# Kernel optimization log

Measured on AMD Instinct MI355X. Metric: run time of the kernel, lower is better.

Reference implementation:

```python
import jax, jax.numpy as jnp
import numpy as np
from jax import lax

B, L, V = 128, 64, 8192
E = H = 128
STEPS = 10
MAX_BIN = 512
BETA_START, BETA_END = 1e-4, 2e-2


def setup_inputs():
    key = jax.random.key(0)
    k = jax.random.split(key, 23)
    s = 0.05
    padded_x = (jax.random.uniform(k[0], (B, L, V)) < 0.01).astype(jnp.float32)
    lengths = jax.random.randint(k[1], (B,), 1, L + 1)
    visit_mask = (jnp.arange(L)[None, :] < lengths[:, None]).astype(jnp.float32)
    padded_bins = jnp.sort(jax.random.randint(k[2], (B, L), 0, MAX_BIN), axis=1)
    t_diff = jax.random.randint(k[3], (B,), 1, STEPS + 1)
    eps = jax.random.normal(k[4], (B, L, E))
    z0 = jax.random.normal(k[5], (B, L, E))
    noise = jax.random.normal(k[6], (STEPS, B, L, E))
    W_visit = jax.random.normal(k[7], (E, V)) * s
    bin_embed = (jax.random.normal(k[8], (MAX_BIN + 2, E)) * s).at[0].set(0.0)  # padding_idx=0
    W_ih = jax.random.normal(k[9], (4 * H, E)) * s
    W_hh = jax.random.normal(k[10], (4 * H, H)) * s
    b_ih = jax.random.normal(k[11], (4 * H,)) * s
    b_hh = jax.random.normal(k[12], (4 * H,)) * s
    W_cls = jax.random.normal(k[13], (1, H)) * s
    b_cls = jax.random.normal(k[14], (1,)) * s
    W_proj = jax.random.normal(k[15], (E, H)) * s
    time_embed = jax.random.normal(k[16], (STEPS + 1, E)) * s
    W_fuse = jax.random.normal(k[17], (2, 2 * E)) * s
    b_fuse = jax.random.normal(k[18], (2,)) * s
    W_e1 = jax.random.normal(k[19], (E, 2 * E)) * s
    b_e1 = jax.random.normal(k[20], (E,)) * s
    W_e2 = jax.random.normal(k[21], (E, E)) * s
    b_e2 = jax.random.normal(k[22], (E,)) * s
    return dict(padded_x=padded_x, visit_mask=visit_mask, padded_bins=padded_bins,
                t_diff=t_diff, eps=eps, z0=z0, noise=noise, W_visit=W_visit,
                bin_embed=bin_embed, W_ih=W_ih, W_hh=W_hh, b_ih=b_ih, b_hh=b_hh,
                W_cls=W_cls, b_cls=b_cls, W_proj=W_proj, time_embed=time_embed,
                W_fuse=W_fuse, b_fuse=b_fuse, W_e1=W_e1, b_e1=b_e1, W_e2=W_e2, b_e2=b_e2)


def _lstm(v, W_ih, W_hh, b_ih, b_hh):
    # v: [B,L,E] -> h: [B,L,H]; PyTorch gate order i,f,g,o
    xg = jnp.einsum('ble,ge->blg', v, W_ih) + b_ih + b_hh
    def step(carry, x):
        h, c = carry
        g = x + h @ W_hh.T
        i, f, gg, o = jnp.split(g, 4, axis=-1)
        c = jax.nn.sigmoid(f) * c + jax.nn.sigmoid(i) * jnp.tanh(gg)
        h = jax.nn.sigmoid(o) * jnp.tanh(c)
        return (h, c), h
    z = jnp.zeros((v.shape[0], W_hh.shape[1]), v.dtype)
    _, hs = lax.scan(step, (z, z), jnp.swapaxes(xg, 0, 1))
    return jnp.swapaxes(hs, 0, 1)


def _last_hidden(h, mask):
    lengths = jnp.maximum(mask.sum(axis=1).astype(jnp.int32), 1)
    return h[jnp.arange(h.shape[0]), lengths - 1]


def reference(padded_x, visit_mask, padded_bins, t_diff, eps, z0, noise,
              W_visit, bin_embed, W_ih, W_hh, b_ih, b_hh, W_cls, b_cls,
              W_proj, time_embed, W_fuse, b_fuse, W_e1, b_e1, W_e2, b_e2):
    m = visit_mask[..., None]                      # [B,L,1]
    betas = jnp.linspace(BETA_START, BETA_END, STEPS)
    alphas = 1.0 - betas
    alpha_bars = jnp.cumprod(alphas)

    # visit embedding + time-gap (delta bin) embedding
    delta = jnp.concatenate([jnp.zeros_like(padded_bins[:, :1]),
                             jnp.clip(padded_bins[:, 1:] - padded_bins[:, :-1], 0)], axis=1)
    delta = jnp.where(visit_mask > 0, jnp.clip(delta, 0, MAX_BIN + 1), 0)
    v = (padded_x @ W_visit.T + bin_embed[delta]) * m  # [B,L,E]

    # encoder LSTM (packed seq == plain scan then zero padded suffix positions)
    h = _lstm(v, W_ih, W_hh, b_ih, b_hh) * m
    logits_real = (_last_hidden(h, visit_mask) @ W_cls.T + b_cls)[:, 0]

    h_prev = jnp.pad(h[:, :-1], ((0, 0), (1, 0), (0, 0)))
    hp = (h_prev @ W_proj.T) * m                   # [B,L,E]

    def fuse_eps(z, t_emb):
        a = jax.nn.softmax(jnp.concatenate([z, hp], -1) @ W_fuse.T + b_fuse, axis=-1)
        g = a[..., :1] * z + a[..., 1:] * hp
        x = jnp.concatenate([g, t_emb], -1)
        return jax.nn.relu(x @ W_e1.T + b_e1) @ W_e2.T + b_e2

    # diffusion loss
    t = jnp.where(visit_mask > 0, t_diff[:, None], 1)    # [B,L]
    ab = alpha_bars[t - 1][..., None]
    z_t = (jnp.sqrt(ab) * v + jnp.sqrt(1.0 - ab) * eps) * m
    eps_pred = fuse_eps(z_t, time_embed[t])
    denom = jnp.maximum(visit_mask.sum(), 1.0)
    diffusion_loss = jnp.sum((eps_pred - eps) ** 2 * m) / denom

    # reverse diffusion sampling of synthetic visit embeddings
    def step(z, inp):
        kk, nz = inp
        t_s = jnp.where(visit_mask > 0, kk, 1)
        e = fuse_eps(z, time_embed[t_s])
        beta = betas[kk - 1]
        mean = (z - beta / jnp.sqrt(1.0 - alpha_bars[kk - 1]) * e) / jnp.sqrt(alphas[kk - 1])
        z = jnp.where(kk > 1, mean + jnp.sqrt(beta) * nz, mean) * m
        return z, None

    ks = jnp.arange(STEPS, 0, -1)
    v_syn, _ = lax.scan(step, z0, (ks, noise))

    h_syn = _lstm(v_syn, W_ih, W_hh, b_ih, b_hh) * m
    logits_syn = (_last_hidden(h_syn, visit_mask) @ W_cls.T + b_cls)[:, 0]
    return logits_real, logits_syn, diffusion_loss
```

## Files before the change

kernel.cpp:

```cpp
#include <hip/hip_runtime.h>

#define B_ 128
#define L_ 64
#define V_ 8192
#define E_ 128
#define H_ 128
#define G4_ 512
#define NROW (B_*L_)
#define HSTRIDE 136
#define AS 136
#define XS 264
#define YS 136
#define ZS 132

typedef unsigned short u16;
typedef __attribute__((ext_vector_type(8))) short bf16x8;
typedef __attribute__((ext_vector_type(4))) float f32x4;

__device__ __forceinline__ float sigm(float x){ return 1.f/(1.f + __expf(-x)); }
__device__ __forceinline__ float ftanh(float x){ float e = __expf(2.f*x); return 1.f - 2.f/(e + 1.f); }
__device__ __forceinline__ u16 f2bf(float f){
    union { unsigned int i; float f; } x; x.f = f;
    unsigned int r = x.i + 0x7fff + ((x.i >> 16) & 1);
    return (u16)(r >> 16);
}
#define LBAR() asm volatile("s_waitcnt lgkmcnt(0)\ns_barrier" ::: "memory")

__device__ __forceinline__ bf16x8 pack8(const float* p){
    const float4* q = (const float4*)p;
    float4 a = q[0], b = q[1];
    bf16x8 f;
    f[0]=(short)f2bf(a.x); f[1]=(short)f2bf(a.y); f[2]=(short)f2bf(a.z); f[3]=(short)f2bf(a.w);
    f[4]=(short)f2bf(b.x); f[5]=(short)f2bf(b.y); f[6]=(short)f2bf(b.z); f[7]=(short)f2bf(b.w);
    return f;
}

__global__ __launch_bounds__(256) void k_transpose_wv(const float* __restrict__ Wv, float* __restrict__ WT){
    __shared__ float tile[16][129];
    int v0 = blockIdx.x * 16;
    int t = threadIdx.x;
    #pragma unroll
    for(int i=0;i<8;i++){
        int idx = i*256 + t; int e = idx >> 4; int vv = idx & 15;
        tile[vv][e] = Wv[(size_t)e*V_ + v0 + vv];
    }
    __syncthreads();
    #pragma unroll
    for(int i=0;i<8;i++){
        int idx = i*256 + t; int vv = idx >> 7; int e = idx & 127;
        WT[(size_t)(v0+vv)*E_ + e] = tile[vv][e];
    }
}

__global__ __launch_bounds__(256) void k_visit_embed(const float* __restrict__ px, const float* __restrict__ vmask,
                                                     const int* __restrict__ bins, const float* __restrict__ bemb,
                                                     const float* __restrict__ WT, float* __restrict__ v){
    __shared__ int idxs[512];
    __shared__ int cnt;
    __shared__ int dsh;
    __shared__ float msh;
    __shared__ float4 red[8][32];
    int row = blockIdx.x; int l = row & 63;
    int t = threadIdx.x;
    if(t==0){
        cnt = 0;
        float m = vmask[row];
        int d = 0;
        if(l > 0){ d = bins[row] - bins[row-1]; d = d < 0 ? 0 : (d > 513 ? 513 : d); }
        if(!(m > 0.f)) d = 0;
        dsh = d; msh = m;
    }
    __syncthreads();
    const uint4* xr4 = (const uint4*)(px + (size_t)row * V_);
    for(int i=t;i<2048;i+=256){
        uint4 u = xr4[i];
        unsigned int w[4] = {u.x,u.y,u.z,u.w};
        #pragma unroll
        for(int j=0;j<4;j++){
            if(w[j]){ int p = atomicAdd(&cnt,1); if(p<512) idxs[p] = i*4 + j; }
        }
    }
    __syncthreads();
    int n = cnt; if(n > 512) n = 512;
    int eq = t & 31, jg = t >> 5;
    float4 a4 = {0.f,0.f,0.f,0.f};
    for(int j=jg;j<n;j+=8){
        const float4* wr = (const float4*)(WT + (size_t)idxs[j]*E_);
        float4 wv = wr[eq];
        a4.x += wv.x; a4.y += wv.y; a4.z += wv.z; a4.w += wv.w;
    }
    red[jg][eq] = a4;
    __syncthreads();
    if(t < 32){
        float4 s = red[0][t];
        #pragma unroll
        for(int g=1;g<8;g++){
            float4 r = red[g][t];
            s.x += r.x; s.y += r.y; s.z += r.z; s.w += r.w;
        }
        const float4* bp = (const float4*)(bemb + dsh*E_);
        float4 bv = bp[t];
        float m = msh;
        float4 o;
        o.x = (s.x + bv.x)*m; o.y = (s.y + bv.y)*m; o.z = (s.z + bv.z)*m; o.w = (s.w + bv.w)*m;
        ((float4*)(v + (size_t)row*E_))[t] = o;
    }
}

__global__ __launch_bounds__(256,2) void k_gemm_xg(const float* __restrict__ A, const float* __restrict__ Wih,
                                                   const float* __restrict__ bih, const float* __restrict__ bhh,
                                                   float* __restrict__ xg){
    __shared__ __align__(16) u16 abuf[16*AS];
    int t = threadIdx.x, wave = t >> 6, lane = t & 63, quad = lane >> 4, lc = lane & 15;
    int row0 = blockIdx.x * 16;
    #pragma unroll
    for(int i=0;i<8;i++){
        int flat = i*256 + t; int r = flat >> 7, e = flat & 127;
        abuf[r*AS + e] = f2bf(A[(size_t)(row0+r)*E_ + e]);
    }
    bf16x8 wfr[8][4]; float bb[8];
    #pragma unroll
    for(int nt=0;nt<8;nt++){
        int n = wave*128 + nt*16 + lc;
        bb[nt] = bih[n] + bhh[n];
        const float* wr = Wih + (size_t)n*E_ + quad*8;
        #pragma unroll
        for(int kt=0;kt<4;kt++) wfr[nt][kt] = pack8(wr + kt*32);
    }
    __syncthreads();
    f32x4 acc[8];
    #pragma unroll
    for(int nt=0;nt<8;nt++) acc[nt] = (f32x4){0.f,0.f,0.f,0.f};
    #pragma unroll
    for(int kt=0;kt<4;kt++){
        bf16x8 af = *(const bf16x8*)&abuf[lc*AS + kt*32 + quad*8];
        #pragma unroll
        for(int nt=0;nt<8;nt++)
            acc[nt] = __builtin_amdgcn_mfma_f32_16x16x32_bf16(af, wfr[nt][kt], acc[nt], 0,0,0);
    }
    #pragma unroll
    for(int nt=0;nt<8;nt++){
        int n = wave*128 + nt*16 + lc;
        #pragma unroll
        for(int r=0;r<4;r++)
            xg[(size_t)(row0 + quad*4 + r)*G4_ + n] = acc[nt][r] + bb[nt];
    }
}

__device__ __forceinline__ void lstm_step(int l, const float* pxg, float* hp_out, bool dohp,
        const u16* bufr, u16* bufw, const bf16x8 (&bf)[4][4], const bf16x8 (&wp)[4],
        float (&xgbuf)[4][4], float (&c4)[4], float (&lg4)[4],
        const int (&len4)[4], float wcv,
        const float* vmsh, int lc, int quad, int wave, int b0){
    float xloc[4][4];
    #pragma unroll
    for(int gate=0;gate<4;gate++){
        #pragma unroll
        for(int r=0;r<4;r++) xloc[gate][r] = xgbuf[gate][r];
    }
    if(l+2 < 64){
        #pragma unroll
        for(int gate=0;gate<4;gate++){
            #pragma unroll
            for(int r=0;r<4;r++)
                xgbuf[gate][r] = pxg[(size_t)r*64*G4_ + (size_t)(l+2)*G4_ + gate*128];
        }
    }
    bf16x8 af[4];
    #pragma unroll
    for(int kt=0;kt<4;kt++)
        af[kt] = *(const bf16x8*)&bufr[lc*HSTRIDE + kt*32 + quad*8];
    f32x4 acc[4], acch;
    #pragma unroll
    for(int a=0;a<4;a++) acc[a] = (f32x4){0.f,0.f,0.f,0.f};
    acch = (f32x4){0.f,0.f,0.f,0.f};
    #pragma unroll
    for(int kt=0;kt<4;kt++){
        #pragma unroll
        for(int a=0;a<4;a++)
            acc[a] = __builtin_amdgcn_mfma_f32_16x16x32_bf16(af[kt], bf[a][kt], acc[a], 0,0,0);
        acch = __builtin_amdgcn_mfma_f32_16x16x32_bf16(af[kt], wp[kt], acch, 0,0,0);
    }
    if(dohp){
        #pragma unroll
        for(int r=0;r<4;r++){
            float m = vmsh[(quad*4+r)*64 + l];
            int grow = (b0 + quad*4 + r)*64 + l;
            hp_out[(size_t)grow*E_ + wave*16 + lc] = acch[r] * m;
        }
    }
    #pragma unroll
    for(int r=0;r<4;r++){
        float gi = acc[0][r] + xloc[0][r];
        float gf = acc[1][r] + xloc[1][r];
        float gg = acc[2][r] + xloc[2][r];
        float go = acc[3][r] + xloc[3][r];
        float c  = sigm(gf)*c4[r] + sigm(gi)*ftanh(gg);
        float h  = sigm(go)*ftanh(c);
        c4[r] = c;
        bufw[(quad*4+r)*HSTRIDE + wave*16 + lc] = f2bf(h);
        if(l == len4[r]-1) lg4[r] += h * wcv;
    }
    LBAR();
}

__global__ __launch_bounds__(512,2) void k_lstm_fused(const float* __restrict__ xg, const float* __restrict__ Whh,
        const float* __restrict__ Wproj, const float* __restrict__ Wcls, const float* __restrict__ bcls,
        const float* __restrict__ vmask, float* __restrict__ hp_out, float* __restrict__ logits_out){
    __shared__ u16 hbuf[2][16*HSTRIDE];
    __shared__ float vmsh[16*64];
    __shared__ int lensh[16];
    __shared__ float lgsh[16][132];
    int t = threadIdx.x;
    int wave = t >> 6, lane = t & 63;
    int quad = lane >> 4, lc = lane & 15;
    int b0 = blockIdx.x * 16;
    bool dohp = (hp_out != nullptr);

    for(int i=t;i<16*HSTRIDE;i+=512) hbuf[0][i] = 0;
    for(int i=t;i<1024;i+=512) vmsh[i] = vmask[b0*64 + i];
    __syncthreads();
    if(t < 16){
        int s = 0;
        #pragma unroll
        for(int i=0;i<64;i++) s += (vmsh[t*64 + i] > 0.f) ? 1 : 0;
        lensh[t] = s < 1 ? 1 : s;
    }

    int cw = wave*16 + lc;
    bf16x8 bf[4][4];
    #pragma unroll
    for(int gate=0;gate<4;gate++){
        int n = gate*128 + cw;
        const float* wr = Whh + (size_t)n*H_ + quad*8;
        #pragma unroll
        for(int kt=0;kt<4;kt++) bf[gate][kt] = pack8(wr + kt*32);
    }
    bf16x8 wp[4];
    {
        const float* wr = Wproj + (size_t)cw*H_ + quad*8;
        #pragma unroll
        for(int kt=0;kt<4;kt++) wp[kt] = pack8(wr + kt*32);
    }
    float wcv = Wcls[cw];

    float c4[4] = {0.f,0.f,0.f,0.f};
    float lg4[4] = {0.f,0.f,0.f,0.f};

    const float* pxg = xg + ((size_t)(b0 + quad*4))*64*G4_ + cw;

    float xgvE[4][4], xgvO[4][4];
    #pragma unroll
    for(int gate=0;gate<4;gate++){
        #pragma unroll
        for(int r=0;r<4;r++){
            xgvE[gate][r] = pxg[(size_t)r*64*G4_ + gate*128];
            xgvO[gate][r] = pxg[(size_t)r*64*G4_ + G4_ + gate*128];
        }
    }
    __syncthreads();
    int len4[4];
    #pragma unroll
    for(int r=0;r<4;r++) len4[r] = lensh[quad*4 + r];

    for(int lb=0;lb<64;lb+=2){
        lstm_step(lb,   pxg, hp_out, dohp, hbuf[0], hbuf[1], bf, wp, xgvE, c4, lg4, len4, wcv, vmsh, lc, quad, wave, b0);
        lstm_step(lb+1, pxg, hp_out, dohp, hbuf[1], hbuf[0], bf, wp, xgvO, c4, lg4, len4, wcv, vmsh, lc, quad, wave, b0);
    }
    #pragma unroll
    for(int r=0;r<4;r++) lgsh[quad*4+r][cw] = lg4[r];
    __syncthreads();
    {
        int row = t >> 5, l32 = t & 31;
        float s = lgsh[row][l32] + lgsh[row][l32+32] + lgsh[row][l32+64] + lgsh[row][l32+96];
        s += __shfl_down(s, 16, 32);
        s += __shfl_down(s, 8, 32);
        s += __shfl_down(s, 4, 32);
        s += __shfl_down(s, 2, 32);
        s += __shfl_down(s, 1, 32);
        if(l32 == 0) logits_out[b0 + row] = s + bcls[0];
    }
}

__global__ __launch_bounds__(256,2) void k_drg(const float* __restrict__ v, const float* __restrict__ hp,
        const float* __restrict__ eps, const int* __restrict__ tdiff, const float* __restrict__ vmask,
        const float* __restrict__ z0, const float* __restrict__ noise, const float* __restrict__ temb,
        const float* __restrict__ Wf, const float* __restrict__ bfu,
        const float* __restrict__ We1, const float* __restrict__ be1,
        const float* __restrict__ We2, const float* __restrict__ be2,
        const float* __restrict__ Wih, const float* __restrict__ bih, const float* __restrict__ bhh,
        float* __restrict__ partial, float* __restrict__ xg2){
    __shared__ float zbuf[16*ZS], hpbuf[16*ZS];
    __shared__ __align__(16) u16 xbuf[16*XS];
    __shared__ __align__(16) u16 y1buf[16*YS];
    __shared__ float wfsh[512];
    __shared__ float ssh[16][2], hpd[16][2];
    __shared__ float mrow[16]; __shared__ int trow[16];
    __shared__ float sbeta[10], sabar[10];
    __shared__ float rb[4];
    int row0 = blockIdx.x * 16; int t = threadIdx.x;
    int wave = t >> 6, lane = t & 63, quad = lane >> 4, lc = lane & 15;

    if(t==0){
        float p = 1.f;
        for(int k=0;k<10;k++){ float b = 1e-4f + (0.02f - 1e-4f)*k/9.f; sbeta[k] = b; p *= (1.f - b); sabar[k] = p; }
    }
    if(t < 16){
        int row = row0 + t; float m = vmask[row];
        mrow[t] = m; trow[t] = (m > 0.f) ? tdiff[row >> 6] : 1;
    }
    for(int i=t;i<512;i+=256) wfsh[i] = Wf[i];
    float z0reg[8];
    #pragma unroll
    for(int i=0;i<8;i++){
        int flat = i*256 + t; int r = flat >> 7; int e = flat & 127;
        z0reg[i] = z0[(size_t)(row0+r)*E_ + e];
    }
    __syncthreads();
    #pragma unroll
    for(int i=0;i<8;i++){
        int flat = i*256 + t; int r = flat >> 7; int e = flat & 127; int row = row0 + r;
        float ab = sabar[trow[r]-1];
        zbuf[r*ZS + e] = (sqrtf(ab)*v[(size_t)row*E_ + e] + sqrtf(1.f - ab)*eps[(size_t)row*E_ + e]) * mrow[r];
        hpbuf[r*ZS + e] = hp[(size_t)row*E_ + e];
    }
    bf16x8 wf1[2][8], wf2[2][4];
    float be1v[2], be2v[2];
    #pragma unroll
    for(int nt=0;nt<2;nt++){
        int n = wave*32 + nt*16 + lc;
        be1v[nt] = be1[n]; be2v[nt] = be2[n];
        const float* w1 = We1 + (size_t)n*256 + quad*8;
        #pragma unroll
        for(int kt=0;kt<8;kt++) wf1[nt][kt] = pack8(w1 + kt*32);
        const float* w2 = We2 + (size_t)n*128 + quad*8;
        #pragma unroll
        for(int kt=0;kt<4;kt++) wf2[nt][kt] = pack8(w2 + kt*32);
    }
    __syncthreads();
    {
        int row = t >> 4, k = (t >> 3) & 1, sub = t & 7;
        float p = 0.f;
        #pragma unroll
        for(int i=0;i<16;i++)
            p += hpbuf[row*ZS + sub*16 + i] * wfsh[k*256 + 128 + sub*16 + i];
        p += __shfl_down(p,4); p += __shfl_down(p,2); p += __shfl_down(p,1);
        if(sub == 0) hpd[row][k] = p + bfu[k];
    }
    LBAR();

    for(int s=0;s<11;s++){
        int kk = 10 - (s - 1);
        float nzreg[2][4];
        if(s >= 1){
            #pragma unroll
            for(int nt=0;nt<2;nt++){
                #pragma unroll
                for(int r=0;r<4;r++)
                    nzreg[nt][r] = noise[((size_t)(s-1)*NROW + row0 + quad*4 + r)*E_ + wave*32 + nt*16 + lc];
            }
        }
        {
            int row = t >> 4, k = (t >> 3) & 1, sub = t & 7;
            float q = 0.f;
            #pragma unroll
            for(int i=0;i<16;i++)
                q += zbuf[row*ZS + sub*16 + i] * wfsh[k*256 + sub*16 + i];
            q += __shfl_down(q,4); q += __shfl_down(q,2); q += __shfl_down(q,1);
            if(sub == 0) ssh[row][k] = q + hpd[row][k];
        }
        LBAR();
        {
            int row = t >> 4, c0 = (t & 15) * 16;
            float s0 = ssh[row][0], s1 = ssh[row][1];
            float a0 = 1.f/(1.f + __expf(s1 - s0)), a1 = 1.f - a0;
            int tt = (s == 0) ? trow[row] : ((mrow[row] > 0.f) ? kk : 1);
            #pragma unroll
            for(int i=0;i<16;i++){
                int c = c0 + i;
                float val = (c < 128) ? (a0*zbuf[row*ZS + c] + a1*hpbuf[row*ZS + c])
                                      : temb[tt*E_ + (c - 128)];
                xbuf[row*XS + c] = f2bf(val);
            }
        }
        LBAR();
        f32x4 acc1[2];
        acc1[0] = (f32x4){0.f,0.f,0.f,0.f}; acc1[1] = (f32x4){0.f,0.f,0.f,0.f};
        #pragma unroll
        for(int kt=0;kt<8;kt++){
            bf16x8 af = *(const bf16x8*)&xbuf[lc*XS + kt*32 + quad*8];
            acc1[0] = __builtin_amdgcn_mfma_f32_16x16x32_bf16(af, wf1[0][kt], acc1[0], 0,0,0);
            acc1[1] = __builtin_amdgcn_mfma_f32_16x16x32_bf16(af, wf1[1][kt], acc1[1], 0,0,0);
        }
        #pragma unroll
        for(int nt=0;nt<2;nt++){
            #pragma unroll
            for(int r=0;r<4;r++)
                y1buf[(quad*4+r)*YS + wave*32 + nt*16 + lc] = f2bf(fmaxf(acc1[nt][r] + be1v[nt], 0.f));
        }
        LBAR();
        f32x4 acc2[2];
        acc2[0] = (f32x4){0.f,0.f,0.f,0.f}; acc2[1] = (f32x4){0.f,0.f,0.f,0.f};
        #pragma unroll
        for(int kt=0;kt<4;kt++){
            bf16x8 af = *(const bf16x8*)&y1buf[lc*YS + kt*32 + quad*8];
            acc2[0] = __builtin_amdgcn_mfma_f32_16x16x32_bf16(af, wf2[0][kt], acc2[0], 0,0,0);
            acc2[1] = __builtin_amdgcn_mfma_f32_16x16x32_bf16(af, wf2[1][kt], acc2[1], 0,0,0);
        }
        if(s == 0){
            float lp = 0.f;
            #pragma unroll
            for(int nt=0;nt<2;nt++){
                int n = wave*32 + nt*16 + lc;
                #pragma unroll
                for(int r=0;r<4;r++){
                    int m = quad*4 + r;
                    float d = (acc2[nt][r] + be2v[nt]) - eps[(size_t)(row0+m)*E_ + n];
                    lp += d*d*mrow[m];
                }
            }
            #pragma unroll
            for(int off=32;off;off>>=1) lp += __shfl_down(lp, off);
            if(lane == 0) rb[wave] = lp;
            LBAR();
            if(t == 0) partial[blockIdx.x] = rb[0]+rb[1]+rb[2]+rb[3];
            #pragma unroll
            for(int i=0;i<8;i++){
                int flat = i*256 + t; int r = flat >> 7; int e = flat & 127;
                zbuf[r*ZS + e] = z0reg[i];
            }
            LBAR();
        } else {
            float beta = sbeta[kk-1];
            float c1 = beta / sqrtf(1.f - sabar[kk-1]);
            float c2 = 1.f / sqrtf(1.f - beta);
            float sb = sqrtf(beta);
            #pragma unroll
            for(int nt=0;nt<2;nt++){
                int n = wave*32 + nt*16 + lc;
                #pragma unroll
                for(int r=0;r<4;r++){
                    int m = quad*4 + r;
                    float e = acc2[nt][r] + be2v[nt];
                    float z = zbuf[m*ZS + n];
                    float mean = (z - c1*e) * c2;
                    float znew = (kk > 1) ? (mean + sb*nzreg[nt][r]) : mean;
                    zbuf[m*ZS + n] = znew * mrow[m];
                }
            }
            LBAR();
        }
    }
    {
        int row = t >> 4, c0 = (t & 15) * 8;
        #pragma unroll
        for(int i=0;i<8;i++)
            xbuf[row*XS + c0 + i] = f2bf(zbuf[row*ZS + c0 + i]);
    }
    bf16x8 wg[8][4]; float bb[8];
    #pragma unroll
    for(int nt=0;nt<8;nt++){
        int n = wave*128 + nt*16 + lc;
        bb[nt] = bih[n] + bhh[n];
        const float* wr = Wih + (size_t)n*E_ + quad*8;
        #pragma unroll
        for(int kt=0;kt<4;kt++) wg[nt][kt] = pack8(wr + kt*32);
    }
    LBAR();
    f32x4 ac[8];
    #pragma unroll
    for(int nt=0;nt<8;nt++) ac[nt] = (f32x4){0.f,0.f,0.f,0.f};
    #pragma unroll
    for(int kt=0;kt<4;kt++){
        bf16x8 af = *(const bf16x8*)&xbuf[lc*XS + kt*32 + quad*8];
        #pragma unroll
        for(int nt=0;nt<8;nt++)
            ac[nt] = __builtin_amdgcn_mfma_f32_16x16x32_bf16(af, wg[nt][kt], ac[nt], 0,0,0);
    }
    #pragma unroll
    for(int nt=0;nt<8;nt++){
        int n = wave*128 + nt*16 + lc;
        #pragma unroll
        for(int r=0;r<4;r++)
            xg2[(size_t)(row0 + quad*4 + r)*G4_ + n] = ac[nt][r] + bb[nt];
    }
}

__global__ void k_finalize(const float* __restrict__ partial, const float* __restrict__ vmask, float* __restrict__ out){
    __shared__ float rb[4], rl[4];
    int t = threadIdx.x;
    float s = 0.f;
    for(int i=t;i<NROW;i+=256) s += vmask[i];
    float ls = 0.f;
    for(int i=t;i<512;i+=256) ls += partial[i];
    #pragma unroll
    for(int off=32;off;off>>=1){ s += __shfl_down(s, off); ls += __shfl_down(ls, off); }
    if((t & 63) == 0){ rb[t >> 6] = s; rl[t >> 6] = ls; }
    __syncthreads();
    if(t == 0){
        float denom = rb[0]+rb[1]+rb[2]+rb[3];
        if(denom < 1.f) denom = 1.f;
        out[256] = (rl[0]+rl[1]+rl[2]+rl[3]) / denom;
    }
}

extern "C" void kernel_launch(void* const* d_in, const int* in_sizes, int n_in,
                              void* d_out, int out_size, void* d_ws, size_t ws_size,
                              hipStream_t stream){
    const float* px    = (const float*)d_in[0];
    const float* vmask = (const float*)d_in[1];
    const int*   bins  = (const int*)d_in[2];
    const int*   tdiff = (const int*)d_in[3];
    const float* eps   = (const float*)d_in[4];
    const float* z0    = (const float*)d_in[5];
    const float* noise = (const float*)d_in[6];
    const float* Wv    = (const float*)d_in[7];
    const float* bemb  = (const float*)d_in[8];
    const float* Wih   = (const float*)d_in[9];
    const float* Whh   = (const float*)d_in[10];
    const float* bih   = (const float*)d_in[11];
    const float* bhh   = (const float*)d_in[12];
    const float* Wcls  = (const float*)d_in[13];
    const float* bcls  = (const float*)d_in[14];
    const float* Wproj = (const float*)d_in[15];
    const float* temb  = (const float*)d_in[16];
    const float* Wf    = (const float*)d_in[17];
    const float* bfu   = (const float*)d_in[18];
    const float* We1   = (const float*)d_in[19];
    const float* be1   = (const float*)d_in[20];
    const float* We2   = (const float*)d_in[21];
    const float* be2   = (const float*)d_in[22];
    float* out = (float*)d_out;

    float* ws      = (float*)d_ws;
    float* WT      = ws;
    float* v       = ws + 1048576;
    float* xg      = ws + 2097152;
    float* hp      = ws + 6291456;
    float* partial = ws + 7340032;

    hipLaunchKernelGGL(k_transpose_wv, dim3(V_/16), dim3(256), 0, stream, Wv, WT);
    hipLaunchKernelGGL(k_visit_embed, dim3(NROW), dim3(256), 0, stream, px, vmask, bins, bemb, WT, v);
    hipLaunchKernelGGL(k_gemm_xg, dim3(NROW/16), dim3(256), 0, stream, v, Wih, bih, bhh, xg);
    hipLaunchKernelGGL(k_lstm_fused, dim3(B_/16), dim3(512), 0, stream,
                       xg, Whh, Wproj, Wcls, bcls, vmask, hp, out);
    hipLaunchKernelGGL(k_drg, dim3(NROW/16), dim3(256), 0, stream,
                       v, hp, eps, tdiff, vmask, z0, noise, temb, Wf, bfu,
                       We1, be1, We2, be2, Wih, bih, bhh, partial, xg);
    hipLaunchKernelGGL(k_lstm_fused, dim3(B_/16), dim3(512), 0, stream,
                       xg, Whh, Wproj, Wcls, bcls, vmask, (float*)nullptr, out + 128);
    hipLaunchKernelGGL(k_finalize, dim3(1), dim3(256), 0, stream, partial, vmask, out);
}
```

Measured before the change: 833.4 us.

## Split LSTM recurrence into 4-sequence blocks and store gate preactivations in bf16

The sequential LSTM kernel now assigns 4 batch sequences per block instead of 16, so it launches 32 blocks instead of 8. Each block still runs the 16-row MFMA, but only quad 0 does the gate math and writes results, leaving 12 of the 16 rows as zero padding. This trades wasted MFMA rows for more parallelism in a latency-bound recurrence. Separately, the input-gate preactivations xg are written and read as bf16 rather than fp32, halving that traffic at some cost in accuracy.

```diff
diff --git a/kernel.cpp b/kernel.cpp
--- a/kernel.cpp
+++ b/kernel.cpp
@@ -23,6 +23,9 @@
     union { unsigned int i; float f; } x; x.f = f;
     unsigned int r = x.i + 0x7fff + ((x.i >> 16) & 1);
     return (u16)(r >> 16);
+}
+__device__ __forceinline__ float bf2f(u16 u){
+    union { unsigned int i; float f; } x; x.i = ((unsigned int)u) << 16; return x.f;
 }
 #define LBAR() asm volatile("s_waitcnt lgkmcnt(0)\ns_barrier" ::: "memory")
 
@@ -109,7 +112,7 @@
 
 __global__ __launch_bounds__(256,2) void k_gemm_xg(const float* __restrict__ A, const float* __restrict__ Wih,
                                                    const float* __restrict__ bih, const float* __restrict__ bhh,
-                                                   float* __restrict__ xg){
+                                                   u16* __restrict__ xg){
     __shared__ __align__(16) u16 abuf[16*AS];
     int t = threadIdx.x, wave = t >> 6, lane = t & 63, quad = lane >> 4, lc = lane & 15;
     int row0 = blockIdx.x * 16;
@@ -143,15 +146,15 @@
         int n = wave*128 + nt*16 + lc;
         #pragma unroll
         for(int r=0;r<4;r++)
-            xg[(size_t)(row0 + quad*4 + r)*G4_ + n] = acc[nt][r] + bb[nt];
-    }
-}
-
-__device__ __forceinline__ void lstm_step(int l, const float* pxg, float* hp_out, bool dohp,
+            xg[(size_t)(row0 + quad*4 + r)*G4_ + n] = f2bf(acc[nt][r] + bb[nt]);
+    }
+}
+
+__device__ __forceinline__ void lstm_step(int l, int b0, const u16* __restrict__ xg, float* hp_out, bool dohp,
         const u16* bufr, u16* bufw, const bf16x8 (&bf)[4][4], const bf16x8 (&wp)[4],
         float (&xgbuf)[4][4], float (&c4)[4], float (&lg4)[4],
         const int (&len4)[4], float wcv,
-        const float* vmsh, int lc, int quad, int wave, int b0){
+        const float* vmsh, int lc, int quad, int cw){
     float xloc[4][4];
     #pragma unroll
     for(int gate=0;gate<4;gate++){
@@ -163,7 +166,7 @@
         for(int gate=0;gate<4;gate++){
             #pragma unroll
             for(int r=0;r<4;r++)
-                xgbuf[gate][r] = pxg[(size_t)r*64*G4_ + (size_t)(l+2)*G4_ + gate*128];
+                xgbuf[gate][r] = bf2f(xg[(size_t)((b0+r)*64 + l+2)*G4_ + gate*128 + cw]);
         }
     }
     bf16x8 af[4];
@@ -181,46 +184,43 @@
             acc[a] = __builtin_amdgcn_mfma_f32_16x16x32_bf16(af[kt], bf[a][kt], acc[a], 0,0,0);
         acch = __builtin_amdgcn_mfma_f32_16x16x32_bf16(af[kt], wp[kt], acch, 0,0,0);
     }
-    if(dohp){
+    if(quad == 0){
         #pragma unroll
         for(int r=0;r<4;r++){
-            float m = vmsh[(quad*4+r)*64 + l];
-            int grow = (b0 + quad*4 + r)*64 + l;
-            hp_out[(size_t)grow*E_ + wave*16 + lc] = acch[r] * m;
-        }
-    }
-    #pragma unroll
-    for(int r=0;r<4;r++){
-        float gi = acc[0][r] + xloc[0][r];
-        float gf = acc[1][r] + xloc[1][r];
-        float gg = acc[2][r] + xloc[2][r];
-        float go = acc[3][r] + xloc[3][r];
-        float c  = sigm(gf)*c4[r] + sigm(gi)*ftanh(gg);
-        float h  = sigm(go)*ftanh(c);
-        c4[r] = c;
-        bufw[(quad*4+r)*HSTRIDE + wave*16 + lc] = f2bf(h);
-        if(l == len4[r]-1) lg4[r] += h * wcv;
+            float m = vmsh[r*64 + l];
+            if(dohp)
+                hp_out[(size_t)((b0+r)*64 + l)*E_ + cw] = acch[r] * m;
+            float gi = acc[0][r] + xloc[0][r];
+            float gf = acc[1][r] + xloc[1][r];
+            float gg = acc[2][r] + xloc[2][r];
+            float go = acc[3][r] + xloc[3][r];
+            float c  = sigm(gf)*c4[r] + sigm(gi)*ftanh(gg);
+            float h  = sigm(go)*ftanh(c);
+            c4[r] = c;
+            bufw[r*HSTRIDE + cw] = f2bf(h);
+            if(l == len4[r]-1) lg4[r] += h * wcv;
+        }
     }
     LBAR();
 }
 
-__global__ __launch_bounds__(512,2) void k_lstm_fused(const float* __restrict__ xg, const float* __restrict__ Whh,
+__global__ __launch_bounds__(512,2) void k_lstm_fused(const u16* __restrict__ xg, const float* __restrict__ Whh,
         const float* __restrict__ Wproj, const float* __restrict__ Wcls, const float* __restrict__ bcls,
         const float* __restrict__ vmask, float* __restrict__ hp_out, float* __restrict__ logits_out){
     __shared__ u16 hbuf[2][16*HSTRIDE];
-    __shared__ float vmsh[16*64];
-    __shared__ int lensh[16];
-    __shared__ float lgsh[16][132];
+    __shared__ float vmsh[4*64];
+    __shared__ int lensh[4];
+    __shared__ float lgsh[4][132];
     int t = threadIdx.x;
     int wave = t >> 6, lane = t & 63;
     int quad = lane >> 4, lc = lane & 15;
-    int b0 = blockIdx.x * 16;
+    int b0 = blockIdx.x * 4;
     bool dohp = (hp_out != nullptr);
 
-    for(int i=t;i<16*HSTRIDE;i+=512) hbuf[0][i] = 0;
-    for(int i=t;i<1024;i+=512) vmsh[i] = vmask[b0*64 + i];
-    __syncthreads();
-    if(t < 16){
+    for(int i=t;i<2*16*HSTRIDE;i+=512) ((u16*)hbuf)[i] = 0;
+    for(int i=t;i<256;i+=512) vmsh[i] = vmask[b0*64 + i];
+    __syncthreads();
+    if(t < 4){
         int s = 0;
         #pragma unroll
         for(int i=0;i<64;i++) s += (vmsh[t*64 + i] > 0.f) ? 1 : 0;
@@ -247,30 +247,30 @@
     float c4[4] = {0.f,0.f,0.f,0.f};
     float lg4[4] = {0.f,0.f,0.f,0.f};
 
-    const float* pxg = xg + ((size_t)(b0 + quad*4))*64*G4_ + cw;
-
     float xgvE[4][4], xgvO[4][4];
     #pragma unroll
     for(int gate=0;gate<4;gate++){
         #pragma unroll
         for(int r=0;r<4;r++){
-            xgvE[gate][r] = pxg[(size_t)r*64*G4_ + gate*128];
-            xgvO[gate][r] = pxg[(size_t)r*64*G4_ + G4_ + gate*128];
+            xgvE[gate][r] = bf2f(xg[(size_t)((b0+r)*64 + 0)*G4_ + gate*128 + cw]);
+            xgvO[gate][r] = bf2f(xg[(size_t)((b0+r)*64 + 1)*G4_ + gate*128 + cw]);
         }
     }
     __syncthreads();
     int len4[4];
     #pragma unroll
-    for(int r=0;r<4;r++) len4[r] = lensh[quad*4 + r];
+    for(int r=0;r<4;r++) len4[r] = lensh[r];
 
     for(int lb=0;lb<64;lb+=2){
-        lstm_step(lb,   pxg, hp_out, dohp, hbuf[0], hbuf[1], bf, wp, xgvE, c4, lg4, len4, wcv, vmsh, lc, quad, wave, b0);
-        lstm_step(lb+1, pxg, hp_out, dohp, hbuf[1], hbuf[0], bf, wp, xgvO, c4, lg4, len4, wcv, vmsh, lc, quad, wave, b0);
-    }
-    #pragma unroll
-    for(int r=0;r<4;r++) lgsh[quad*4+r][cw] = lg4[r];
-    __syncthreads();
-    {
+        lstm_step(lb,   b0, xg, hp_out, dohp, hbuf[0], hbuf[1], bf, wp, xgvE, c4, lg4, len4, wcv, vmsh, lc, quad, cw);
+        lstm_step(lb+1, b0, xg, hp_out, dohp, hbuf[1], hbuf[0], bf, wp, xgvO, c4, lg4, len4, wcv, vmsh, lc, quad, cw);
+    }
+    if(quad == 0){
+        #pragma unroll
+        for(int r=0;r<4;r++) lgsh[r][cw] = lg4[r];
+    }
+    __syncthreads();
+    if(t < 128){
         int row = t >> 5, l32 = t & 31;
         float s = lgsh[row][l32] + lgsh[row][l32+32] + lgsh[row][l32+64] + lgsh[row][l32+96];
         s += __shfl_down(s, 16, 32);
@@ -289,7 +289,7 @@
         const float* __restrict__ We1, const float* __restrict__ be1,
         const float* __restrict__ We2, const float* __restrict__ be2,
         const float* __restrict__ Wih, const float* __restrict__ bih, const float* __restrict__ bhh,
-        float* __restrict__ partial, float* __restrict__ xg2){
+        float* __restrict__ partial, u16* __restrict__ xg2){
     __shared__ float zbuf[16*ZS], hpbuf[16*ZS];
     __shared__ __align__(16) u16 xbuf[16*XS];
     __shared__ __align__(16) u16 y1buf[16*YS];
@@ -482,7 +482,7 @@
         int n = wave*128 + nt*16 + lc;
         #pragma unroll
         for(int r=0;r<4;r++)
-            xg2[(size_t)(row0 + quad*4 + r)*G4_ + n] = ac[nt][r] + bb[nt];
+            xg2[(size_t)(row0 + quad*4 + r)*G4_ + n] = f2bf(ac[nt][r] + bb[nt]);
     }
 }
 
@@ -535,19 +535,19 @@
     float* ws      = (float*)d_ws;
     float* WT      = ws;
     float* v       = ws + 1048576;
-    float* xg      = ws + 2097152;
-    float* hp      = ws + 6291456;
-    float* partial = ws + 7340032;
+    u16*   xg      = (u16*)(ws + 2097152);
+    float* hp      = ws + 4194304;
+    float* partial = ws + 5242880;
 
     hipLaunchKernelGGL(k_transpose_wv, dim3(V_/16), dim3(256), 0, stream, Wv, WT);
     hipLaunchKernelGGL(k_visit_embed, dim3(NROW), dim3(256), 0, stream, px, vmask, bins, bemb, WT, v);
     hipLaunchKernelGGL(k_gemm_xg, dim3(NROW/16), dim3(256), 0, stream, v, Wih, bih, bhh, xg);
-    hipLaunchKernelGGL(k_lstm_fused, dim3(B_/16), dim3(512), 0, stream,
+    hipLaunchKernelGGL(k_lstm_fused, dim3(B_/4), dim3(512), 0, stream,
                        xg, Whh, Wproj, Wcls, bcls, vmask, hp, out);
     hipLaunchKernelGGL(k_drg, dim3(NROW/16), dim3(256), 0, stream,
                        v, hp, eps, tdiff, vmask, z0, noise, temb, Wf, bfu,
                        We1, be1, We2, be2, Wih, bih, bhh, partial, xg);
-    hipLaunchKernelGGL(k_lstm_fused, dim3(B_/16), dim3(512), 0, stream,
+    hipLaunchKernelGGL(k_lstm_fused, dim3(B_/4), dim3(512), 0, stream,
                        xg, Whh, Wproj, Wcls, bcls, vmask, (float*)nullptr, out + 128);
     hipLaunchKernelGGL(k_finalize, dim3(1), dim3(256), 0, stream, partial, vmask, out);
 }
```

After: 880.4 us. +5.6%, slower.

## Interleave two independent LSTM chains per block to hide recurrence latency

Applied to the files above, without the earlier changes.

Each LSTM block now handles 32 batch rows as two independent 16-row recurrences whose steps are interleaved, sharing one barrier per timestep pair. The goal is to overlap the MFMA, gate math and LDS latency of one chain with the other, cutting the number of barriers per sequence step. In exchange the grid shrinks from 8 to 4 blocks, so fewer CUs are used, and register pressure rises (launch bounds drop to one block per CU).

```diff
diff --git a/kernel.cpp b/kernel.cpp
--- a/kernel.cpp
+++ b/kernel.cpp
@@ -147,11 +147,11 @@
     }
 }
 
-__device__ __forceinline__ void lstm_step(int l, const float* pxg, float* hp_out, bool dohp,
+__device__ __forceinline__ void chain_step(int l, const float* pxg, float* hp_out, bool dohp,
         const u16* bufr, u16* bufw, const bf16x8 (&bf)[4][4], const bf16x8 (&wp)[4],
         float (&xgbuf)[4][4], float (&c4)[4], float (&lg4)[4],
         const int (&len4)[4], float wcv,
-        const float* vmsh, int lc, int quad, int wave, int b0){
+        const float* vmsh, int lc, int quad, int cw, int base){
     float xloc[4][4];
     #pragma unroll
     for(int gate=0;gate<4;gate++){
@@ -181,16 +181,13 @@
             acc[a] = __builtin_amdgcn_mfma_f32_16x16x32_bf16(af[kt], bf[a][kt], acc[a], 0,0,0);
         acch = __builtin_amdgcn_mfma_f32_16x16x32_bf16(af[kt], wp[kt], acch, 0,0,0);
     }
-    if(dohp){
-        #pragma unroll
-        for(int r=0;r<4;r++){
-            float m = vmsh[(quad*4+r)*64 + l];
-            int grow = (b0 + quad*4 + r)*64 + l;
-            hp_out[(size_t)grow*E_ + wave*16 + lc] = acch[r] * m;
-        }
-    }
     #pragma unroll
     for(int r=0;r<4;r++){
+        float m = vmsh[(quad*4+r)*64 + l];
+        if(dohp){
+            int grow = (base + quad*4 + r)*64 + l;
+            hp_out[(size_t)grow*E_ + cw] = acch[r] * m;
+        }
         float gi = acc[0][r] + xloc[0][r];
         float gf = acc[1][r] + xloc[1][r];
         float gg = acc[2][r] + xloc[2][r];
@@ -198,29 +195,29 @@
         float c  = sigm(gf)*c4[r] + sigm(gi)*ftanh(gg);
         float h  = sigm(go)*ftanh(c);
         c4[r] = c;
-        bufw[(quad*4+r)*HSTRIDE + wave*16 + lc] = f2bf(h);
+        bufw[(quad*4+r)*HSTRIDE + cw] = f2bf(h);
         if(l == len4[r]-1) lg4[r] += h * wcv;
     }
-    LBAR();
-}
-
-__global__ __launch_bounds__(512,2) void k_lstm_fused(const float* __restrict__ xg, const float* __restrict__ Whh,
+}
+
+__global__ __launch_bounds__(512,1) void k_lstm_fused(const float* __restrict__ xg, const float* __restrict__ Whh,
         const float* __restrict__ Wproj, const float* __restrict__ Wcls, const float* __restrict__ bcls,
         const float* __restrict__ vmask, float* __restrict__ hp_out, float* __restrict__ logits_out){
-    __shared__ u16 hbuf[2][16*HSTRIDE];
-    __shared__ float vmsh[16*64];
-    __shared__ int lensh[16];
-    __shared__ float lgsh[16][132];
+    __shared__ u16 hbuf[2][2][16*HSTRIDE];
+    __shared__ float vmsh[32*64];
+    __shared__ int lensh[32];
+    __shared__ float lgsh[32][132];
     int t = threadIdx.x;
     int wave = t >> 6, lane = t & 63;
     int quad = lane >> 4, lc = lane & 15;
-    int b0 = blockIdx.x * 16;
+    int b0 = blockIdx.x * 32;
     bool dohp = (hp_out != nullptr);
 
-    for(int i=t;i<16*HSTRIDE;i+=512) hbuf[0][i] = 0;
-    for(int i=t;i<1024;i+=512) vmsh[i] = vmask[b0*64 + i];
-    __syncthreads();
-    if(t < 16){
+    for(int i=t;i<2*16*HSTRIDE;i+=512){ hbuf[0][0][i>=16*HSTRIDE ? i-16*HSTRIDE : i] = 0; }
+    for(int i=t;i<16*HSTRIDE;i+=512){ hbuf[0][0][i] = 0; hbuf[1][0][i] = 0; }
+    for(int i=t;i<2048;i+=512) vmsh[i] = vmask[b0*64 + i];
+    __syncthreads();
+    if(t < 32){
         int s = 0;
         #pragma unroll
         for(int i=0;i<64;i++) s += (vmsh[t*64 + i] > 0.f) ? 1 : 0;
@@ -244,41 +241,52 @@
     }
     float wcv = Wcls[cw];
 
-    float c4[4] = {0.f,0.f,0.f,0.f};
-    float lg4[4] = {0.f,0.f,0.f,0.f};
-
-    const float* pxg = xg + ((size_t)(b0 + quad*4))*64*G4_ + cw;
-
-    float xgvE[4][4], xgvO[4][4];
+    float c4P[4] = {0,0,0,0}, c4Q[4] = {0,0,0,0};
+    float lgP[4] = {0,0,0,0}, lgQ[4] = {0,0,0,0};
+
+    const float* pxgP = xg + ((size_t)(b0 + quad*4))*64*G4_ + cw;
+    const float* pxgQ = xg + ((size_t)(b0 + 16 + quad*4))*64*G4_ + cw;
+
+    float xPE[4][4], xPO[4][4], xQE[4][4], xQO[4][4];
     #pragma unroll
     for(int gate=0;gate<4;gate++){
         #pragma unroll
         for(int r=0;r<4;r++){
-            xgvE[gate][r] = pxg[(size_t)r*64*G4_ + gate*128];
-            xgvO[gate][r] = pxg[(size_t)r*64*G4_ + G4_ + gate*128];
-        }
-    }
-    __syncthreads();
-    int len4[4];
-    #pragma unroll
-    for(int r=0;r<4;r++) len4[r] = lensh[quad*4 + r];
+            xPE[gate][r] = pxgP[(size_t)r*64*G4_ + gate*128];
+            xPO[gate][r] = pxgP[(size_t)r*64*G4_ + G4_ + gate*128];
+            xQE[gate][r] = pxgQ[(size_t)r*64*G4_ + gate*128];
+            xQO[gate][r] = pxgQ[(size_t)r*64*G4_ + G4_ + gate*128];
+        }
+    }
+    __syncthreads();
+    int lenP[4], lenQ[4];
+    #pragma unroll
+    for(int r=0;r<4;r++){ lenP[r] = lensh[quad*4 + r]; lenQ[r] = lensh[16 + quad*4 + r]; }
 
     for(int lb=0;lb<64;lb+=2){
-        lstm_step(lb,   pxg, hp_out, dohp, hbuf[0], hbuf[1], bf, wp, xgvE, c4, lg4, len4, wcv, vmsh, lc, quad, wave, b0);
-        lstm_step(lb+1, pxg, hp_out, dohp, hbuf[1], hbuf[0], bf, wp, xgvO, c4, lg4, len4, wcv, vmsh, lc, quad, wave, b0);
-    }
-    #pragma unroll
-    for(int r=0;r<4;r++) lgsh[quad*4+r][cw] = lg4[r];
+        chain_step(lb,   pxgP, hp_out, dohp, hbuf[0][0], hbuf[0][1], bf, wp, xPE, c4P, lgP, lenP, wcv, vmsh,        lc, quad, cw, b0);
+        chain_step(lb,   pxgQ, hp_out, dohp, hbuf[1][0], hbuf[1][1], bf, wp, xQE, c4Q, lgQ, lenQ, wcv, vmsh + 1024, lc, quad, cw, b0 + 16);
+        LBAR();
+        chain_step(lb+1, pxgP, hp_out, dohp, hbuf[0][1], hbuf[0][0], bf, wp, xPO, c4P, lgP, lenP, wcv, vmsh,        lc, quad, cw, b0);
+        chain_step(lb+1, pxgQ, hp_out, dohp, hbuf[1][1], hbuf[1][0], bf, wp, xQO, c4Q, lgQ, lenQ, wcv, vmsh + 1024, lc, quad, cw, b0 + 16);
+        LBAR();
+    }
+    #pragma unroll
+    for(int r=0;r<4;r++){
+        lgsh[quad*4 + r][cw] = lgP[r];
+        lgsh[16 + quad*4 + r][cw] = lgQ[r];
+    }
     __syncthreads();
     {
-        int row = t >> 5, l32 = t & 31;
-        float s = lgsh[row][l32] + lgsh[row][l32+32] + lgsh[row][l32+64] + lgsh[row][l32+96];
-        s += __shfl_down(s, 16, 32);
-        s += __shfl_down(s, 8, 32);
-        s += __shfl_down(s, 4, 32);
-        s += __shfl_down(s, 2, 32);
-        s += __shfl_down(s, 1, 32);
-        if(l32 == 0) logits_out[b0 + row] = s + bcls[0];
+        int row = t >> 4, c16 = t & 15;
+        float s = 0.f;
+        #pragma unroll
+        for(int j=0;j<8;j++) s += lgsh[row][c16 + j*16];
+        s += __shfl_down(s, 8);
+        s += __shfl_down(s, 4);
+        s += __shfl_down(s, 2);
+        s += __shfl_down(s, 1);
+        if(c16 == 0) logits_out[b0 + row] = s + bcls[0];
     }
 }
 
@@ -542,12 +550,12 @@
     hipLaunchKernelGGL(k_transpose_wv, dim3(V_/16), dim3(256), 0, stream, Wv, WT);
     hipLaunchKernelGGL(k_visit_embed, dim3(NROW), dim3(256), 0, stream, px, vmask, bins, bemb, WT, v);
     hipLaunchKernelGGL(k_gemm_xg, dim3(NROW/16), dim3(256), 0, stream, v, Wih, bih, bhh, xg);
-    hipLaunchKernelGGL(k_lstm_fused, dim3(B_/16), dim3(512), 0, stream,
+    hipLaunchKernelGGL(k_lstm_fused, dim3(B_/32), dim3(512), 0, stream,
                        xg, Whh, Wproj, Wcls, bcls, vmask, hp, out);
     hipLaunchKernelGGL(k_drg, dim3(NROW/16), dim3(256), 0, stream,
                        v, hp, eps, tdiff, vmask, z0, noise, temb, Wf, bfu,
                        We1, be1, We2, be2, Wih, bih, bhh, partial, xg);
-    hipLaunchKernelGGL(k_lstm_fused, dim3(B_/16), dim3(512), 0, stream,
+    hipLaunchKernelGGL(k_lstm_fused, dim3(B_/32), dim3(512), 0, stream,
                        xg, Whh, Wproj, Wcls, bcls, vmask, (float*)nullptr, out + 128);
     hipLaunchKernelGGL(k_finalize, dim3(1), dim3(256), 0, stream, partial, vmask, out);
 }
```

Measured after the change: 1.138 ms. +36.5%, slower.
